# Kernel tuning notes

Hardware: AMD Instinct MI355X
Metric: run time of the kernel (lower is better)

## Reference

```python
import jax, jax.numpy as jnp
import numpy as np

B, N, M, L, H = 32, 4096, 256, 128, 4
GAMMA = 2.0


def setup_inputs() -> dict:
    key = jax.random.key(0)
    kx, km, kv, ku, kw = jax.random.split(key, 5)
    x = jax.random.normal(kx, (B, N, M), dtype=jnp.float32)
    masks = (jax.random.uniform(km, (B, N)) > 0.3).astype(jnp.float32)
    # VarianceScaling(scale=0.1, fan_in, uniform) ~ small init; exact dist doesn't affect math
    V = jax.random.normal(kv, (H, M, L), dtype=jnp.float32) * 0.02
    U = jax.random.normal(ku, (H, M, L), dtype=jnp.float32) * 0.02
    w = jax.random.normal(kw, (H, L, 1), dtype=jnp.float32) * 0.05
    return {"x": x, "masks": masks, "V": V, "U": U, "w": w}


def reference(x, masks, V, U, w):
    # x: [B,N,M], masks: [B,N], V/U: [H,M,L], w: [H,L,1]
    m = masks[:, None, :, None]  # [B,1,N,1] broadcast over heads
    gated = jnp.tanh(jnp.einsum('bnm,hml->bhnl', x, V)) * jax.nn.sigmoid(
        jnp.einsum('bnm,hml->bhnl', x, U))          # [B,H,N,L]
    logits = jnp.einsum('bhnl,hl->bhn', gated, w[..., 0])[..., None]  # [B,H,N,1]
    a = m * logits                                   # masked logits (as in original)
    a = m * jnp.exp(a)                               # masked exp
    a = a / jnp.sum(a, axis=2, keepdims=True)        # softmax over instances
    ag = a ** GAMMA
    a = ag / jnp.sum(ag, axis=2, keepdims=True)      # gamma-power renorm
    emb = jnp.einsum('bhnk,bnm->bhm', a, x)          # weighted sum; k is the trailing 1
    emb = emb.reshape(B, H * M)                      # concat heads along axis=1
    att = jnp.transpose(a, (1, 0, 2, 3))             # [H,B,N,1] (per-head attention list)
    return (att, emb)
```

## Files before the change

### kernel.cpp

```cpp
#include <hip/hip_runtime.h>
#include <hip/hip_bf16.h>
#include <stdint.h>

#define B_ 32
#define N_ 4096
#define M_ 256
#define L_ 128
#define H_ 4
#define BN_ (B_ * N_)

typedef __bf16 bf16x8 __attribute__((ext_vector_type(8)));
typedef float  f32x4  __attribute__((ext_vector_type(4)));

__device__ __forceinline__ unsigned short f2bf(float f) {
    unsigned int u = __float_as_uint(f);
    u += 0x7fffu + ((u >> 16) & 1u);
    return (unsigned short)(u >> 16);
}
__device__ __forceinline__ unsigned int pack2(float lo, float hi) {
    return (unsigned int)f2bf(lo) | ((unsigned int)f2bf(hi) << 16);
}

__device__ __forceinline__ void gload16(const void* g, void* l) {
    __builtin_amdgcn_global_load_lds(
        (const __attribute__((address_space(1))) unsigned int*)g,
        (__attribute__((address_space(3))) unsigned int*)l, 16, 0, 0);
}

__global__ void prep_vu_img2(const float* __restrict__ V, const float* __restrict__ U,
                             unsigned short* __restrict__ vu) {
    __shared__ float slab[64][129];
    const int b   = blockIdx.x;
    const int mat = b & 1, ks = (b >> 1) & 3, h = b >> 3;
    const float* src = (mat ? U : V) + ((size_t)h * M_ + ks * 64) * L_;
    const float scale = mat ? -1.0f : 2.0f;
    const int tid = threadIdx.x;
#pragma unroll
    for (int rep = 0; rep < 32; ++rep) {
        int idx = rep * 256 + tid;
        slab[idx >> 7][idx & 127] = scale * src[(size_t)(idx >> 7) * L_ + (idx & 127)];
    }
    __syncthreads();
#pragma unroll
    for (int rep = 0; rep < 4; ++rep) {
        int cidx = rep * 256 + tid;
        int l  = cidx >> 3;
        int kk = (cidx & 7) * 8;
        uint4 o;
        o.x = pack2(slab[kk + 0][l], slab[kk + 1][l]);
        o.y = pack2(slab[kk + 2][l], slab[kk + 3][l]);
        o.z = pack2(slab[kk + 4][l], slab[kk + 5][l]);
        o.w = pack2(slab[kk + 6][l], slab[kk + 7][l]);
        int tl = kk >> 5, kl = kk & 31;
        int lh = l >> 6, ll = l & 63;
        char* dst = (char*)vu
            + ((((size_t)(h * 2 + lh) * 8 + (ks * 2 + tl)) * 2) + mat) * 4096;
        int byte = (ll * 64 + kl * 2) ^ ((ll & 14) << 3);
        *(uint4*)(dst + byte) = o;
    }
}

__global__ __launch_bounds__(256, 4)
void gemm_fast13(const float* __restrict__ x,
                 const unsigned short* __restrict__ vu,
                 const float* __restrict__ w,
                 float* __restrict__ partL) {
    __shared__ __align__(16) float          xs[4096];
    __shared__ __align__(16) unsigned short vs[2][2048];
    __shared__ __align__(16) unsigned short us[2][2048];

    const int orig    = blockIdx.x;
    const int logical = (orig & 7) * 1024 + (orig >> 3);
    const int tile    = logical >> 3;
    const int h       = (logical >> 1) & 3;
    const int lh      = logical & 1;

    const int tid  = threadIdx.x;
    const int lane = tid & 63;
    const int wv   = tid >> 6;
    const int g    = lane >> 4;
    const int c    = lane & 15;

    f32x4 accV[2][4], accU[2][4];
#pragma unroll
    for (int rf = 0; rf < 2; ++rf)
#pragma unroll
        for (int cf = 0; cf < 4; ++cf) {
            accV[rf][cf] = (f32x4){0.f, 0.f, 0.f, 0.f};
            accU[rf][cf] = (f32x4){0.f, 0.f, 0.f, 0.f};
        }

    const char* gvs = (const char*)vu + (size_t)(h * 2 + lh) * 65536
                      + wv * 1024 + lane * 16;
    const char* gus = gvs + 4096;

    const int offb = ((lane & 7) << 4) ^ (((lane >> 3) & 6) << 3);
    const size_t rowbase = (size_t)tile * 128 + wv * 32 + (lane >> 3);
    const char* px0 = (const char*)x + (rowbase +  0) * 1024 + offb;
    const char* px1 = (const char*)x + (rowbase +  8) * 1024 + (offb ^ 64);
    const char* px2 = (const char*)x + (rowbase + 16) * 1024 + offb;
    const char* px3 = (const char*)x + (rowbase + 24) * 1024 + (offb ^ 64);

    int aoff[2], boff[4];
#pragma unroll
    for (int rf = 0; rf < 2; ++rf) {
        int r = wv * 32 + rf * 16 + c;
        aoff[rf] = (r * 128 + g * 32) ^ ((r & 14) << 3);
    }
#pragma unroll
    for (int cf = 0; cf < 4; ++cf) {
        int ll = cf * 16 + c;
        boff[cf] = (ll * 64 + g * 16) ^ ((ll & 14) << 3);
    }

#define SCHED __builtin_amdgcn_sched_barrier(0)

#define STAGEX(t) do {                                                   \
        char* _d = (char*)xs + wv * 4096;                                \
        gload16(px0 + (t) * 128, _d);                                    \
        gload16(px1 + (t) * 128, _d + 1024);                             \
        gload16(px2 + (t) * 128, _d + 2048);                             \
        gload16(px3 + (t) * 128, _d + 3072);                             \
    } while (0)

#define STAGEB(t, bufi) do {                                             \
        gload16(gvs + (t) * 8192, (char*)vs[bufi] + wv * 1024);          \
        gload16(gus + (t) * 8192, (char*)us[bufi] + wv * 1024);          \
    } while (0)

    STAGEX(0);
    STAGEB(0, 0);
    SCHED;

#pragma unroll
    for (int t = 0; t < 8; ++t) {
        asm volatile("s_waitcnt vmcnt(0)" ::: "memory");
        __builtin_amdgcn_s_barrier();
        SCHED;

        bf16x8 a0, a1;
        {
            f32x4 p = *(const f32x4*)((const char*)xs + aoff[0]);
            f32x4 q = *(const f32x4*)((const char*)xs + (aoff[0] ^ 16));
            a0[0] = (__bf16)p.x; a0[1] = (__bf16)p.y;
            a0[2] = (__bf16)p.z; a0[3] = (__bf16)p.w;
            a0[4] = (__bf16)q.x; a0[5] = (__bf16)q.y;
            a0[6] = (__bf16)q.z; a0[7] = (__bf16)q.w;
            p = *(const f32x4*)((const char*)xs + aoff[1]);
            q = *(const f32x4*)((const char*)xs + (aoff[1] ^ 16));
            a1[0] = (__bf16)p.x; a1[1] = (__bf16)p.y;
            a1[2] = (__bf16)p.z; a1[3] = (__bf16)p.w;
            a1[4] = (__bf16)q.x; a1[5] = (__bf16)q.y;
            a1[6] = (__bf16)q.z; a1[7] = (__bf16)q.w;
        }

        if (t < 7) {
            asm volatile("s_waitcnt lgkmcnt(0)" ::: "memory");
            SCHED;
            STAGEX(t + 1);
            STAGEB(t + 1, (t + 1) & 1);
            SCHED;
        }

        const int buf = t & 1;
        const char* vbuf = (const char*)vs[buf];
        const char* ubuf = (const char*)us[buf];

        __builtin_amdgcn_s_setprio(1);
#pragma unroll
        for (int cf = 0; cf < 4; ++cf) {
            bf16x8 bv = *(const bf16x8*)(vbuf + boff[cf]);
            bf16x8 bu = *(const bf16x8*)(ubuf + boff[cf]);
            accV[0][cf] = __builtin_amdgcn_mfma_f32_16x16x32_bf16(a0, bv, accV[0][cf], 0, 0, 0);
            accV[1][cf] = __builtin_amdgcn_mfma_f32_16x16x32_bf16(a1, bv, accV[1][cf], 0, 0, 0);
            accU[0][cf] = __builtin_amdgcn_mfma_f32_16x16x32_bf16(a0, bu, accU[0][cf], 0, 0, 0);
            accU[1][cf] = __builtin_amdgcn_mfma_f32_16x16x32_bf16(a1, bu, accU[1][cf], 0, 0, 0);
        }
        __builtin_amdgcn_s_setprio(0);
    }
#undef STAGEB
#undef STAGEX
#undef SCHED

    const float* wrow = w + h * L_ + lh * 64;
    float* pl = partL + (size_t)lh * (B_ * H_ * N_);
#pragma unroll
    for (int rf = 0; rf < 2; ++rf) {
        float plog[4] = {0.f, 0.f, 0.f, 0.f};
#pragma unroll
        for (int cf = 0; cf < 4; ++cf) {
            float wvv = wrow[cf * 16 + c];
#pragma unroll
            for (int i = 0; i < 4; ++i) {
                float A = __expf(accV[rf][cf][i]);
                float E = __expf(accU[rf][cf][i]);
                float gg = __fdividef(A - 1.f, (A + 1.f) * (1.f + E));
                plog[i] += gg * wvv;
            }
        }
#pragma unroll
        for (int i = 0; i < 4; ++i) {
            float v = plog[i];
            v += __shfl_xor(v, 1);
            v += __shfl_xor(v, 2);
            v += __shfl_xor(v, 4);
            v += __shfl_xor(v, 8);
            if (c == 0) {
                int rowflat = tile * 128 + wv * 32 + rf * 16 + g * 4 + i;
                int b = rowflat >> 12;
                int n = rowflat & (N_ - 1);
                pl[((size_t)b * H_ + h) * N_ + n] = v;
            }
        }
    }
}

__global__ void prep_vu_slow(const float* __restrict__ V, const float* __restrict__ U,
                             unsigned short* __restrict__ Vt, unsigned short* __restrict__ Ut) {
    int idx = blockIdx.x * 256 + threadIdx.x;
    int m = idx & (M_ - 1);
    int l = (idx >> 8) & (L_ - 1);
    int h = idx >> 15;
    Vt[idx] = f2bf(V[((size_t)h * M_ + m) * L_ + l]);
    Ut[idx] = f2bf(U[((size_t)h * M_ + m) * L_ + l]);
}

#define BM 128
#define BK 64

__global__ __launch_bounds__(256, 2)
void gemm_logits(const float* __restrict__ x,
                 const unsigned short* __restrict__ Vt,
                 const unsigned short* __restrict__ Ut,
                 const float* __restrict__ w,
                 float* __restrict__ logits) {
    __shared__ __align__(16) unsigned short xs[BM * BK];
    __shared__ __align__(16) unsigned short vs[L_ * BK];
    __shared__ __align__(16) unsigned short us[L_ * BK];
    __shared__ float wl[L_];

    const int h    = blockIdx.x >> 10;
    const int tile = blockIdx.x & 1023;
    const int row0 = tile * BM;
    const int tid  = threadIdx.x;
    const int lane = tid & 63;
    const int wave = tid >> 6;

    if (tid < L_) wl[tid] = w[h * L_ + tid];

    f32x4 accV[2][8], accU[2][8];
#pragma unroll
    for (int rf = 0; rf < 2; ++rf)
#pragma unroll
        for (int cf = 0; cf < 8; ++cf) {
            accV[rf][cf] = (f32x4){0.f, 0.f, 0.f, 0.f};
            accU[rf][cf] = (f32x4){0.f, 0.f, 0.f, 0.f};
        }

    const unsigned short* Vh = Vt + (size_t)h * L_ * M_;
    const unsigned short* Uh = Ut + (size_t)h * L_ * M_;
    const int g = lane >> 4;
    const int c = lane & 15;

    for (int ks = 0; ks < 4; ++ks) {
        const int k0 = ks * BK;
        __syncthreads();
#pragma unroll
        for (int p = 0; p < 4; ++p) {
            int row = p * 32 + (tid >> 3);
            int kk  = (tid & 7) * 8;
            const float* gx = x + (size_t)(row0 + row) * M_ + k0 + kk;
            float4 a = *(const float4*)gx;
            float4 b = *(const float4*)(gx + 4);
            uint4 o;
            o.x = pack2(a.x, a.y); o.y = pack2(a.z, a.w);
            o.z = pack2(b.x, b.y); o.w = pack2(b.z, b.w);
            int byte = (row * BK + kk) * 2;
            byte ^= (row & 7) << 4;
            *(uint4*)((char*)xs + byte) = o;
        }
#pragma unroll
        for (int p = 0; p < 4; ++p) {
            int l  = p * 32 + (tid >> 3);
            int kk = (tid & 7) * 8;
            uint4 v = *(const uint4*)(Vh + (size_t)l * M_ + k0 + kk);
            uint4 u = *(const uint4*)(Uh + (size_t)l * M_ + k0 + kk);
            int byte = (l * BK + kk) * 2;
            byte ^= (l & 7) << 4;
            *(uint4*)((char*)vs + byte) = v;
            *(uint4*)((char*)us + byte) = u;
        }
        __syncthreads();
#pragma unroll
        for (int ksub = 0; ksub < 2; ++ksub) {
            bf16x8 afr[2];
#pragma unroll
            for (int rf = 0; rf < 2; ++rf) {
                int row = wave * 32 + rf * 16 + c;
                int byte = (row * BK + ksub * 32 + g * 8) * 2;
                byte ^= (row & 7) << 4;
                afr[rf] = *(const bf16x8*)((const char*)xs + byte);
            }
#pragma unroll
            for (int cf = 0; cf < 8; ++cf) {
                int l = cf * 16 + c;
                int byte = (l * BK + ksub * 32 + g * 8) * 2;
                byte ^= (l & 7) << 4;
                bf16x8 bv = *(const bf16x8*)((const char*)vs + byte);
                bf16x8 bu = *(const bf16x8*)((const char*)us + byte);
#pragma unroll
                for (int rf = 0; rf < 2; ++rf) {
                    accV[rf][cf] = __builtin_amdgcn_mfma_f32_16x16x32_bf16(afr[rf], bv, accV[rf][cf], 0, 0, 0);
                    accU[rf][cf] = __builtin_amdgcn_mfma_f32_16x16x32_bf16(afr[rf], bu, accU[rf][cf], 0, 0, 0);
                }
            }
        }
    }
#pragma unroll
    for (int rf = 0; rf < 2; ++rf) {
        float plog[4] = {0.f, 0.f, 0.f, 0.f};
#pragma unroll
        for (int cf = 0; cf < 8; ++cf) {
            float wvv = wl[cf * 16 + c];
#pragma unroll
            for (int i = 0; i < 4; ++i) {
                float vv = accV[rf][cf][i];
                float uu = accU[rf][cf][i];
                vv = fminf(fmaxf(vv, -20.f), 20.f);
                float e2v = __expf(2.f * vv);
                float t = __fdividef(e2v - 1.f, e2v + 1.f);
                float s = __fdividef(1.f, 1.f + __expf(-uu));
                plog[i] += t * s * wvv;
            }
        }
#pragma unroll
        for (int i = 0; i < 4; ++i) {
            float v = plog[i];
            v += __shfl_xor(v, 1);
            v += __shfl_xor(v, 2);
            v += __shfl_xor(v, 4);
            v += __shfl_xor(v, 8);
            if (c == 0) {
                int rowflat = row0 + wave * 32 + rf * 16 + g * 4 + i;
                int b = rowflat >> 12;
                int n = rowflat & (N_ - 1);
                logits[((size_t)b * H_ + h) * N_ + n] = v;
            }
        }
    }
}

__global__ __launch_bounds__(256)
void softmax_att2(const float* __restrict__ pl0, const float* __restrict__ pl1,
                  const float* __restrict__ masks, float* __restrict__ att) {
    const int bh = blockIdx.x;
    const int b = bh >> 2, h = bh & 3;
    __shared__ float e2s[N_];
    __shared__ float red[4];
    const int tid = threadIdx.x;

    float sum = 0.f;
#pragma unroll
    for (int i = 0; i < N_ / 256; ++i) {
        int n = i * 256 + tid;
        size_t idx = ((size_t)b * H_ + h) * N_ + n;
        float lg = pl0[idx] + pl1[idx];
        float mv = masks[(size_t)b * N_ + n];
        float e = mv * __expf(mv * lg);
        float e2 = e * e;
        e2s[n] = e2;
        sum += e2;
    }
#pragma unroll
    for (int off = 32; off >= 1; off >>= 1) sum += __shfl_xor(sum, off);
    if ((tid & 63) == 0) red[tid >> 6] = sum;
    __syncthreads();
    float S = red[0] + red[1] + red[2] + red[3];
    float inv = 1.f / S;
#pragma unroll
    for (int i = 0; i < N_ / 256; ++i) {
        int n = i * 256 + tid;
        att[((size_t)h * B_ + b) * N_ + n] = e2s[n] * inv;
    }
}

__global__ __launch_bounds__(256)
void softmax_att(const float* __restrict__ logits, const float* __restrict__ masks,
                 float* __restrict__ att) {
    const int bh = blockIdx.x;
    const int b = bh >> 2, h = bh & 3;
    __shared__ float e2s[N_];
    __shared__ float red[4];
    const int tid = threadIdx.x;

    float sum = 0.f;
#pragma unroll
    for (int i = 0; i < N_ / 256; ++i) {
        int n = i * 256 + tid;
        float lg = logits[((size_t)b * H_ + h) * N_ + n];
        float mv = masks[(size_t)b * N_ + n];
        float e = mv * __expf(mv * lg);
        float e2 = e * e;
        e2s[n] = e2;
        sum += e2;
    }
#pragma unroll
    for (int off = 32; off >= 1; off >>= 1) sum += __shfl_xor(sum, off);
    if ((tid & 63) == 0) red[tid >> 6] = sum;
    __syncthreads();
    float S = red[0] + red[1] + red[2] + red[3];
    float inv = 1.f / S;
#pragma unroll
    for (int i = 0; i < N_ / 256; ++i) {
        int n = i * 256 + tid;
        att[((size_t)h * B_ + b) * N_ + n] = e2s[n] * inv;
    }
}

#define NCH 32
#define CHUNK (N_ / NCH)

__global__ __launch_bounds__(256)
void emb_partial(const float* __restrict__ x, const float* __restrict__ att,
                 float* __restrict__ part) {
    const int bc = blockIdx.x;
    const int b = bc >> 5, ch = bc & 31;
    __shared__ float as[H_][CHUNK];
    const int tid = threadIdx.x;

    for (int i = tid; i < H_ * CHUNK; i += 256) {
        int hh = i >> 7;
        int j  = i & (CHUNK - 1);
        as[hh][j] = att[((size_t)hh * B_ + b) * N_ + ch * CHUNK + j];
    }
    __syncthreads();

    float a0 = 0.f, a1 = 0.f, a2 = 0.f, a3 = 0.f;
    const float* xp = x + ((size_t)b * N_ + ch * CHUNK) * M_ + tid;
#pragma unroll 4
    for (int j = 0; j < CHUNK; ++j) {
        float xv = xp[(size_t)j * M_];
        a0 += as[0][j] * xv;
        a1 += as[1][j] * xv;
        a2 += as[2][j] * xv;
        a3 += as[3][j] * xv;
    }
    float* pp = part + (size_t)bc * H_ * M_ + tid;
    pp[0 * M_] = a0; pp[1 * M_] = a1; pp[2 * M_] = a2; pp[3 * M_] = a3;
}

__global__ __launch_bounds__(256)
void emb_reduce(const float* __restrict__ part, float* __restrict__ emb) {
    int idx = blockIdx.x * 256 + threadIdx.x;
    int b = idx >> 10;
    int r = idx & 1023;
    float s = 0.f;
#pragma unroll
    for (int ci = 0; ci < NCH; ++ci)
        s += part[((size_t)(b * NCH + ci)) * (H_ * M_) + r];
    emb[idx] = s;
}

extern "C" void kernel_launch(void* const* d_in, const int* in_sizes, int n_in,
                              void* d_out, int out_size, void* d_ws, size_t ws_size,
                              hipStream_t stream) {
    const float* x     = (const float*)d_in[0];
    const float* masks = (const float*)d_in[1];
    const float* V     = (const float*)d_in[2];
    const float* U     = (const float*)d_in[3];
    const float* w     = (const float*)d_in[4];

    float* att = (float*)d_out;
    float* emb = att + (size_t)H_ * B_ * N_;

    char* ws = (char*)d_ws;
    const size_t VU_BYTES  = (size_t)128 * 4096;
    const size_t PL_BYTES  = (size_t)2 * B_ * H_ * N_ * 4;
    const size_t PT_BYTES  = (size_t)B_ * NCH * H_ * M_ * 4;
    const size_t NEED_FAST = VU_BYTES + PL_BYTES + PT_BYTES;

    if (ws_size >= NEED_FAST) {
        unsigned short* vuimg = (unsigned short*)ws;
        float* partL = (float*)(ws + VU_BYTES);
        float* partp = (float*)(ws + VU_BYTES + PL_BYTES);

        prep_vu_img2<<<32,   256, 0, stream>>>(V, U, vuimg);
        gemm_fast13 <<<8192, 256, 0, stream>>>(x, vuimg, w, partL);
        softmax_att2<<<B_ * H_, 256, 0, stream>>>(partL,
                                                  partL + (size_t)B_ * H_ * N_,
                                                  masks, att);
        emb_partial<<<B_ * NCH, 256, 0, stream>>>(x, att, partp);
        emb_reduce <<<(B_ * H_ * M_) / 256, 256, 0, stream>>>(partp, emb);
    } else {
        unsigned short* Vt = (unsigned short*)ws;
        unsigned short* Ut = (unsigned short*)(ws + 262144);
        float* logits = (float*)(ws + 524288);
        float* partp  = (float*)(ws + 524288 + (size_t)B_ * H_ * N_ * 4);

        prep_vu_slow<<<512, 256, 0, stream>>>(V, U, Vt, Ut);
        gemm_logits <<<4096, 256, 0, stream>>>(x, Vt, Ut, w, logits);
        softmax_att <<<B_ * H_, 256, 0, stream>>>(logits, masks, att);
        emb_partial <<<B_ * NCH, 256, 0, stream>>>(x, att, partp);
        emb_reduce  <<<(B_ * H_ * M_) / 256, 256, 0, stream>>>(partp, emb);
    }
}
```

Before: 151.4 us.

## Triple-buffer x and V/U staging in logits GEMM with two-ahead prefetch

The logits GEMM previously had a single x buffer and double V/U buffers, so every iteration drained all outstanding global loads before computing. It now keeps three LDS buffers for x, V and U, prefetches two k-steps ahead, and waits with vmcnt(6) so one stage's loads stay in flight during compute. This raises LDS per block to about 72KB, and launch bounds drop from 4 to 2 blocks per CU, trading occupancy for deeper per-block latency hiding. The explicit lgkmcnt wait before overwriting a buffer is also removed, relying on the barrier alone to separate reads of the previous stage from the next async LDS write.

```diff
diff --git a/kernel.cpp b/kernel.cpp
--- a/kernel.cpp
+++ b/kernel.cpp
@@ -60,14 +60,14 @@
     }
 }
 
-__global__ __launch_bounds__(256, 4)
-void gemm_fast13(const float* __restrict__ x,
+__global__ __launch_bounds__(256, 2)
+void gemm_fast15(const float* __restrict__ x,
                  const unsigned short* __restrict__ vu,
                  const float* __restrict__ w,
                  float* __restrict__ partL) {
-    __shared__ __align__(16) float          xs[4096];
-    __shared__ __align__(16) unsigned short vs[2][2048];
-    __shared__ __align__(16) unsigned short us[2][2048];
+    __shared__ __align__(16) float          xs[3][4096];
+    __shared__ __align__(16) unsigned short vs[3][2048];
+    __shared__ __align__(16) unsigned short us[3][2048];
 
     const int orig    = blockIdx.x;
     const int logical = (orig & 7) * 1024 + (orig >> 3);
@@ -115,71 +115,67 @@
 
 #define SCHED __builtin_amdgcn_sched_barrier(0)
 
-#define STAGEX(t) do {                                                   \
-        char* _d = (char*)xs + wv * 4096;                                \
+#define STAGE(t, bufi) do {                                              \
+        char* _d = (char*)xs[bufi] + wv * 4096;                          \
         gload16(px0 + (t) * 128, _d);                                    \
         gload16(px1 + (t) * 128, _d + 1024);                             \
         gload16(px2 + (t) * 128, _d + 2048);                             \
         gload16(px3 + (t) * 128, _d + 3072);                             \
-    } while (0)
-
-#define STAGEB(t, bufi) do {                                             \
         gload16(gvs + (t) * 8192, (char*)vs[bufi] + wv * 1024);          \
         gload16(gus + (t) * 8192, (char*)us[bufi] + wv * 1024);          \
     } while (0)
 
-    STAGEX(0);
-    STAGEB(0, 0);
+#define COMPUTE(BI) do {                                                 \
+        const char* _xb = (const char*)xs[BI];                           \
+        const char* _vb = (const char*)vs[BI];                           \
+        const char* _ub = (const char*)us[BI];                           \
+        bf16x8 a0, a1;                                                   \
+        {                                                                \
+            f32x4 p = *(const f32x4*)(_xb + aoff[0]);                    \
+            f32x4 q = *(const f32x4*)(_xb + (aoff[0] ^ 16));             \
+            a0[0] = (__bf16)p.x; a0[1] = (__bf16)p.y;                    \
+            a0[2] = (__bf16)p.z; a0[3] = (__bf16)p.w;                    \
+            a0[4] = (__bf16)q.x; a0[5] = (__bf16)q.y;                    \
+            a0[6] = (__bf16)q.z; a0[7] = (__bf16)q.w;                    \
+            p = *(const f32x4*)(_xb + aoff[1]);                          \
+            q = *(const f32x4*)(_xb + (aoff[1] ^ 16));                   \
+            a1[0] = (__bf16)p.x; a1[1] = (__bf16)p.y;                    \
+            a1[2] = (__bf16)p.z; a1[3] = (__bf16)p.w;                    \
+            a1[4] = (__bf16)q.x; a1[5] = (__bf16)q.y;                    \
+            a1[6] = (__bf16)q.z; a1[7] = (__bf16)q.w;                    \
+        }                                                                \
+        __builtin_amdgcn_s_setprio(1);                                   \
+        _Pragma("unroll")                                                \
+        for (int cf = 0; cf < 4; ++cf) {                                 \
+            bf16x8 bv = *(const bf16x8*)(_vb + boff[cf]);                \
+            bf16x8 bu = *(const bf16x8*)(_ub + boff[cf]);                \
+            accV[0][cf] = __builtin_amdgcn_mfma_f32_16x16x32_bf16(a0, bv, accV[0][cf], 0, 0, 0); \
+            accV[1][cf] = __builtin_amdgcn_mfma_f32_16x16x32_bf16(a1, bv, accV[1][cf], 0, 0, 0); \
+            accU[0][cf] = __builtin_amdgcn_mfma_f32_16x16x32_bf16(a0, bu, accU[0][cf], 0, 0, 0); \
+            accU[1][cf] = __builtin_amdgcn_mfma_f32_16x16x32_bf16(a1, bu, accU[1][cf], 0, 0, 0); \
+        }                                                                \
+        __builtin_amdgcn_s_setprio(0);                                   \
+    } while (0)
+
+    STAGE(0, 0);
     SCHED;
+    STAGE(1, 1);
+    SCHED;
 
 #pragma unroll
     for (int t = 0; t < 8; ++t) {
-        asm volatile("s_waitcnt vmcnt(0)" ::: "memory");
+        if (t < 7) asm volatile("s_waitcnt vmcnt(6)" ::: "memory");
+        else       asm volatile("s_waitcnt vmcnt(0)" ::: "memory");
         __builtin_amdgcn_s_barrier();
         SCHED;
 
-        bf16x8 a0, a1;
-        {
-            f32x4 p = *(const f32x4*)((const char*)xs + aoff[0]);
-            f32x4 q = *(const f32x4*)((const char*)xs + (aoff[0] ^ 16));
-            a0[0] = (__bf16)p.x; a0[1] = (__bf16)p.y;
-            a0[2] = (__bf16)p.z; a0[3] = (__bf16)p.w;
-            a0[4] = (__bf16)q.x; a0[5] = (__bf16)q.y;
-            a0[6] = (__bf16)q.z; a0[7] = (__bf16)q.w;
-            p = *(const f32x4*)((const char*)xs + aoff[1]);
-            q = *(const f32x4*)((const char*)xs + (aoff[1] ^ 16));
-            a1[0] = (__bf16)p.x; a1[1] = (__bf16)p.y;
-            a1[2] = (__bf16)p.z; a1[3] = (__bf16)p.w;
-            a1[4] = (__bf16)q.x; a1[5] = (__bf16)q.y;
-            a1[6] = (__bf16)q.z; a1[7] = (__bf16)q.w;
-        }
-
-        if (t < 7) {
-            asm volatile("s_waitcnt lgkmcnt(0)" ::: "memory");
-            SCHED;
-            STAGEX(t + 1);
-            STAGEB(t + 1, (t + 1) & 1);
-            SCHED;
-        }
-
-        const int buf = t & 1;
-        const char* vbuf = (const char*)vs[buf];
-        const char* ubuf = (const char*)us[buf];
-
-        __builtin_amdgcn_s_setprio(1);
-#pragma unroll
-        for (int cf = 0; cf < 4; ++cf) {
-            bf16x8 bv = *(const bf16x8*)(vbuf + boff[cf]);
-            bf16x8 bu = *(const bf16x8*)(ubuf + boff[cf]);
-            accV[0][cf] = __builtin_amdgcn_mfma_f32_16x16x32_bf16(a0, bv, accV[0][cf], 0, 0, 0);
-            accV[1][cf] = __builtin_amdgcn_mfma_f32_16x16x32_bf16(a1, bv, accV[1][cf], 0, 0, 0);
-            accU[0][cf] = __builtin_amdgcn_mfma_f32_16x16x32_bf16(a0, bu, accU[0][cf], 0, 0, 0);
-            accU[1][cf] = __builtin_amdgcn_mfma_f32_16x16x32_bf16(a1, bu, accU[1][cf], 0, 0, 0);
-        }
-        __builtin_amdgcn_s_setprio(0);
-    }
-#undef STAGEB
-#undef STAGEX
+        if (t < 6) STAGE(t + 2, (t + 2) % 3);
+        SCHED;
+
+        COMPUTE(t % 3);
+    }
+#undef COMPUTE
+#undef STAGE
 #undef SCHED
 
     const float* wrow = w + h * L_ + lh * 64;
@@ -485,7 +481,7 @@
         float* partp = (float*)(ws + VU_BYTES + PL_BYTES);
 
         prep_vu_img2<<<32,   256, 0, stream>>>(V, U, vuimg);
-        gemm_fast13 <<<8192, 256, 0, stream>>>(x, vuimg, w, partL);
+        gemm_fast15 <<<8192, 256, 0, stream>>>(x, vuimg, w, partL);
         softmax_att2<<<B_ * H_, 256, 0, stream>>>(partL,
                                                   partL + (size_t)B_ * H_ * N_,
                                                   masks, att);
```

After: 187.9 us. 24.1% more time.
